# Kernel optimization log

Hardware: AMD Instinct MI355X
Metric: run time of the kernel (lower is better)

Reference implementation:

```python
import jax, jax.numpy as jnp
from jax import lax
import numpy as np

B, C, H, W = 1, 128, 32, 32
OC, K = 128, 3
STRIDE, PAD, DIL = 1, 1, 1
ARRAY_SIZE = 32
QUANT = 8


def setup_inputs() -> dict:
    key = jax.random.key(0)
    k1, k2, k3 = jax.random.split(key, 3)
    x = jax.random.normal(k1, (B, C, H, W), dtype=jnp.float32)
    weight = jax.random.normal(k2, (OC, C, K, K), dtype=jnp.float32) * 0.05
    bias = jax.random.normal(k3, (OC,), dtype=jnp.float32) * 0.05
    return {"x": x, "weight": weight, "bias": bias}


def _conv(x, w, b):
    out = lax.conv_general_dilated(
        x, w, window_strides=(STRIDE, STRIDE),
        padding=((PAD, PAD), (PAD, PAD)),
        rhs_dilation=(DIL, DIL),
        dimension_numbers=("NCHW", "OIHW", "NCHW"))
    return out + b[None, :, None, None]


def _unfold(x, oh, ow):
    # torch F.unfold: (B, C*K*K, L) with channel-major ordering (c, kh, kw)
    xp = jnp.pad(x, ((0, 0), (0, 0), (PAD, PAD), (PAD, PAD)))
    cols = jnp.stack(
        [xp[:, :, i:i + oh, j:j + ow] for i in range(K) for j in range(K)],
        axis=2)  # (B, C, K*K, OH, OW)
    return cols.reshape(B, C * K * K, oh * ow)


def reference(x, weight, bias):
    oh = (H + 2 * PAD - DIL * (K - 1) - 1) // STRIDE + 1
    ow = (W + 2 * PAD - DIL * (K - 1) - 1) // STRIDE + 1
    L = oh * ow
    qmax = float(2 ** QUANT - 1)

    # --- set_quant_params: per-spatial-location scale/zero_point from full conv out ---
    out_full = _conv(x, weight, bias).reshape(1, OC, -1)  # (1, OC, L)
    mx = jnp.max(out_full, axis=1)  # (1, L)
    mn = jnp.min(out_full, axis=1)
    scale = (mx - mn) / qmax
    zp = jnp.clip(-mn / scale, 0.0, qmax)
    zp = jnp.where(jnp.isnan(zp), 0.0, zp)
    zp = jnp.trunc(zp)  # .int() truncation
    scale = lax.stop_gradient(scale)[:, None, None, :]  # (1,1,1,L)
    zp = lax.stop_gradient(zp)[:, None, None, :]

    # --- unfold + explicit elementwise multiply (crossbar expansion) ---
    cols = _unfold(x, oh, ow)                       # (B, C*K*K, L)
    pre = cols[:, None, :, :] * weight.reshape(1, OC, C * K * K, 1)  # (B,OC,CKK,L)

    # pad front of dim 2 to a multiple of array_size (pads a full chunk if divisible)
    ckk = C * K * K
    pad_d3 = ARRAY_SIZE - ckk % ARRAY_SIZE
    pre = jnp.pad(pre, ((0, 0), (0, 0), (pad_d3, 0), (0, 0)))

    # block-sum over array_size chunks (crossbar partial sums)
    n_chunks = (ckk + pad_d3) // ARRAY_SIZE
    accu = pre.reshape(B, OC, n_chunks, ARRAY_SIZE, L).sum(axis=3)  # (B,OC,n_chunks,L)

    # per-chunk fake-quant (Quant8F) with straight-through estimator
    q = jnp.clip(jnp.round(accu / scale) + zp, 0.0, qmax)
    deq = (q - zp) * scale
    quant_accu = accu + lax.stop_gradient(deq - accu)

    # reduce over chunks -> conv output (note: bias is NOT added in original forward)
    return quant_accu.sum(axis=2).reshape(B, OC, oh, ow)
```

## Files before the change

### kernel.cpp

```cpp
#include <hip/hip_runtime.h>

#define L_     1024
#define CKK_   1152
#define QMAX_  255.0f
#define NCH    36
#define PLANE_ 131072

__global__ __launch_bounds__(256) void gemm_chunks(
    const float* __restrict__ x,
    const float* __restrict__ w,
    float* __restrict__ planes)
{
    __shared__ __align__(16) float Ws[8][32];
    const int t      = threadIdx.x;
    const int ocBase = blockIdx.x * 8;
    const int l      = blockIdx.y * 256 + t;
    const int j      = blockIdx.z;
    const int oh     = l >> 5, ow = l & 31;
    const int d0     = j * 32;

    const int  s_oc = t >> 5, s_k = t & 31;
    const float wval = w[(ocBase + s_oc) * CKK_ + d0 + s_k];

    float xv[32];
#pragma unroll
    for (int dd = 0; dd < 32; dd++) {
        const int d  = d0 + dd;
        const int c  = d / 9;
        const int r  = d - 9 * c;
        const int kh = r / 3;
        const int kw = r - 3 * kh;
        const int off = c * 1024 + (kh - 1) * 32 + (kw - 1);
        const bool ok = ((unsigned)(oh + kh - 1) < 32u) &
                        ((unsigned)(ow + kw - 1) < 32u);
        const int idx = ok ? (off + l) : 0;
        const float vv = x[idx];
        xv[dd] = ok ? vv : 0.f;
    }

    Ws[s_oc][s_k] = wval;
    __syncthreads();

    float acc[8];
#pragma unroll
    for (int oc = 0; oc < 8; oc++) {
        const float4* wp = (const float4*)&Ws[oc][0];
        float pa = 0.f, pb = 0.f;
#pragma unroll
        for (int k4 = 0; k4 < 4; k4++) {
            const float4 wv = wp[k4];
            pa = fmaf(wv.x, xv[4 * k4 + 0], pa);
            pa = fmaf(wv.y, xv[4 * k4 + 1], pa);
            pa = fmaf(wv.z, xv[4 * k4 + 2], pa);
            pa = fmaf(wv.w, xv[4 * k4 + 3], pa);
        }
#pragma unroll
        for (int k4 = 4; k4 < 8; k4++) {
            const float4 wv = wp[k4];
            pb = fmaf(wv.x, xv[4 * k4 + 0], pb);
            pb = fmaf(wv.y, xv[4 * k4 + 1], pb);
            pb = fmaf(wv.z, xv[4 * k4 + 2], pb);
            pb = fmaf(wv.w, xv[4 * k4 + 3], pb);
        }
        acc[oc] = pa + pb;
    }

    float* dst = planes + (size_t)j * PLANE_ + (size_t)l * 128 + ocBase;
    *(float4*)(dst + 0) = make_float4(acc[0], acc[1], acc[2], acc[3]);
    *(float4*)(dst + 4) = make_float4(acc[4], acc[5], acc[6], acc[7]);
}

__global__ __launch_bounds__(256) void fused_mq(
    const float* __restrict__ planes,
    const float* __restrict__ bias,
    float* __restrict__ out)
{
    __shared__ float part[256];
    __shared__ float mnb[128], mxb[128];
    __shared__ float s_sc, s_zp, s_iv;
    const int t  = threadIdx.x;
    const int oc = t & 127, jh = t >> 7;
    const int l  = blockIdx.x;

    const float* p = planes + (size_t)(jh * 18) * PLANE_ + (size_t)l * 128 + oc;
    float v[18];
#pragma unroll
    for (int j = 0; j < 18; j++) v[j] = p[(size_t)j * PLANE_];

    float s = 0.f;
#pragma unroll
    for (int j = 0; j < 18; j++) s += v[j];
    part[t] = s;
    __syncthreads();

    if (t < 128) {
        const float tot = part[t] + part[t + 128] + bias[t];
        mnb[t] = tot;
        mxb[t] = tot;
    }
    __syncthreads();
#pragma unroll
    for (int st = 64; st > 0; st >>= 1) {
        if (t < st) {
            mnb[t] = fminf(mnb[t], mnb[t + st]);
            mxb[t] = fmaxf(mxb[t], mxb[t + st]);
        }
        __syncthreads();
    }
    if (t == 0) {
        const float amn = mnb[0], amx = mxb[0];
        const float sv  = (amx - amn) / QMAX_;
        float z = -amn / sv;
        z = fmaxf(z, 0.f);
        z = fminf(z, QMAX_);
        z = truncf(z);
        s_sc = sv;
        s_zp = z;
        s_iv = 1.0f / sv;
    }
    __syncthreads();

    const float sc = s_sc, zv = s_zp, iv = s_iv;
    float q = 0.f;
#pragma unroll
    for (int j = 0; j < 18; j++) {
        float qn = rintf(v[j] * iv) + zv;
        qn = fminf(fmaxf(qn, 0.f), QMAX_);
        q += (qn - zv) * sc;
    }
    part[t] = q;
    __syncthreads();

    if (t < 128)
        out[oc * L_ + l] = part[t] + part[t + 128];
}

template <bool QUANT>
__global__ __launch_bounds__(256) void cas_direct(
    const float* __restrict__ x, const float* __restrict__ w,
    float* __restrict__ out, const float* __restrict__ scale,
    const float* __restrict__ zp, const float* __restrict__ inv)
{
    const int t = threadIdx.x;
    const int ocBase = blockIdx.x * 16;
    const int l = blockIdx.y * 256 + t;
    const int oh = l >> 5, ow = l & 31;

    float sc = 0.f, zv = 0.f, iv = 0.f;
    if (QUANT) { sc = scale[l]; zv = zp[l]; iv = inv[l]; }

    float acc[16];
#pragma unroll
    for (int oc = 0; oc < 16; oc++) acc[oc] = 0.f;

    for (int j = 0; j < NCH; j++) {
        const int d0 = j * 32;
        float xv[32];
#pragma unroll
        for (int dd = 0; dd < 32; dd++) {
            const int d = d0 + dd, c = d / 9, r = d - 9 * c;
            const int kh = r / 3, kw = r - 3 * kh;
            const int off = c * 1024 + (kh - 1) * 32 + (kw - 1);
            const bool ok = ((unsigned)(oh + kh - 1) < 32u) &
                            ((unsigned)(ow + kw - 1) < 32u);
            const int idx = ok ? (off + l) : 0;
            const float vv = x[idx];
            xv[dd] = ok ? vv : 0.f;
        }
#pragma unroll
        for (int oc = 0; oc < 16; oc++) {
            const float4* wp = (const float4*)(w + (ocBase + oc) * CKK_ + d0);
            float pa = 0.f, pb = 0.f;
#pragma unroll
            for (int k4 = 0; k4 < 8; k4++) {
                const float4 wv = wp[k4];
                float& pr = (k4 < 4) ? pa : pb;
                pr = fmaf(wv.x, xv[4 * k4 + 0], pr);
                pr = fmaf(wv.y, xv[4 * k4 + 1], pr);
                pr = fmaf(wv.z, xv[4 * k4 + 2], pr);
                pr = fmaf(wv.w, xv[4 * k4 + 3], pr);
            }
            const float s2 = pa + pb;
            if (QUANT) {
                float qn = rintf(s2 * iv) + zv;
                qn = fminf(fmaxf(qn, 0.f), QMAX_);
                acc[oc] += (qn - zv) * sc;
            } else {
                acc[oc] += s2;
            }
        }
    }
#pragma unroll
    for (int oc = 0; oc < 16; oc++)
        out[(ocBase + oc) * L_ + l] = acc[oc];
}

__global__ __launch_bounds__(256) void minmax_conv(
    const float* __restrict__ conv, const float* __restrict__ bias,
    float* __restrict__ scale, float* __restrict__ zp, float* __restrict__ inv)
{
    __shared__ float smn[16][17], smx[16][17];
    const int t = threadIdx.x, li = t & 15, g = t >> 4;
    const int l = blockIdx.x * 16 + li;
    float mn = INFINITY, mx = -INFINITY;
#pragma unroll
    for (int i = 0; i < 8; i++) {
        const int oc = g * 8 + i;
        const float v = conv[oc * L_ + l] + bias[oc];
        mn = fminf(mn, v); mx = fmaxf(mx, v);
    }
    smn[g][li] = mn; smx[g][li] = mx;
    __syncthreads();
    if (t < 16) {
        const int l2 = blockIdx.x * 16 + t;
        float amn = smn[0][t], amx = smx[0][t];
#pragma unroll
        for (int g2 = 1; g2 < 16; g2++) {
            amn = fminf(amn, smn[g2][t]); amx = fmaxf(amx, smx[g2][t]);
        }
        const float s = (amx - amn) / QMAX_;
        float z = -amn / s;
        z = fminf(fmaxf(z, 0.f), QMAX_);
        z = truncf(z);
        scale[l2] = s; zp[l2] = z; inv[l2] = 1.0f / s;
    }
}

extern "C" void kernel_launch(void* const* d_in, const int* in_sizes, int n_in,
                              void* d_out, int out_size, void* d_ws, size_t ws_size,
                              hipStream_t stream) {
    const float* x    = (const float*)d_in[0];
    const float* w    = (const float*)d_in[1];
    const float* bias = (const float*)d_in[2];
    float* out = (float*)d_out;
    float* ws  = (float*)d_ws;

    const size_t main_need = (size_t)NCH * PLANE_ * 4;
    if (ws_size >= main_need) {
        float* planes = ws;
        gemm_chunks<<<dim3(16, 4, NCH), 256, 0, stream>>>(x, w, planes);
        fused_mq<<<1024, 256, 0, stream>>>(planes, bias, out);
    } else {
        float* conv  = ws;
        float* scale = conv + PLANE_;
        float* zpv   = scale + 1024;
        float* inv   = zpv + 1024;
        cas_direct<false><<<dim3(8, 4), 256, 0, stream>>>(x, w, conv, nullptr, nullptr, nullptr);
        minmax_conv<<<64, 256, 0, stream>>>(conv, bias, scale, zpv, inv);
        cas_direct<true><<<dim3(8, 4), 256, 0, stream>>>(x, w, out, scale, zpv, inv);
    }
}
```

Baseline: 82.38 us.

## Retile chunk GEMM with shared-memory x and weight tiles and register blocking

The per-chunk GEMM kernel now stages a 32x128 weight slice (transposed) and a 32x64 im2col tile of x in shared memory. Each thread computes a 4x8 register tile of output channels by spatial positions. Previously every block re-gathered 32 x values per thread for only 8 output channels, so x reads and address math were repeated across 16 oc-blocks. The new layout cuts redundant global gathers and raises FMA-to-load ratio. The cost is fewer, larger blocks (576 vs 2304) and more shared memory per block.

New measurement: 75.92 us. 7.8% less time.

```diff
diff --git a/kernel.cpp b/kernel.cpp
--- a/kernel.cpp
+++ b/kernel.cpp
@@ -11,63 +11,107 @@
     const float* __restrict__ w,
     float* __restrict__ planes)
 {
-    __shared__ __align__(16) float Ws[8][32];
-    const int t      = threadIdx.x;
-    const int ocBase = blockIdx.x * 8;
-    const int l      = blockIdx.y * 256 + t;
-    const int j      = blockIdx.z;
-    const int oh     = l >> 5, ow = l & 31;
-    const int d0     = j * 32;
-
-    const int  s_oc = t >> 5, s_k = t & 31;
-    const float wval = w[(ocBase + s_oc) * CKK_ + d0 + s_k];
-
-    float xv[32];
-#pragma unroll
-    for (int dd = 0; dd < 32; dd++) {
-        const int d  = d0 + dd;
-        const int c  = d / 9;
-        const int r  = d - 9 * c;
-        const int kh = r / 3;
-        const int kw = r - 3 * kh;
-        const int off = c * 1024 + (kh - 1) * 32 + (kw - 1);
-        const bool ok = ((unsigned)(oh + kh - 1) < 32u) &
-                        ((unsigned)(ow + kw - 1) < 32u);
-        const int idx = ok ? (off + l) : 0;
-        const float vv = x[idx];
-        xv[dd] = ok ? vv : 0.f;
-    }
-
-    Ws[s_oc][s_k] = wval;
-    __syncthreads();
-
-    float acc[8];
-#pragma unroll
-    for (int oc = 0; oc < 8; oc++) {
-        const float4* wp = (const float4*)&Ws[oc][0];
-        float pa = 0.f, pb = 0.f;
-#pragma unroll
-        for (int k4 = 0; k4 < 4; k4++) {
-            const float4 wv = wp[k4];
-            pa = fmaf(wv.x, xv[4 * k4 + 0], pa);
-            pa = fmaf(wv.y, xv[4 * k4 + 1], pa);
-            pa = fmaf(wv.z, xv[4 * k4 + 2], pa);
-            pa = fmaf(wv.w, xv[4 * k4 + 3], pa);
-        }
-#pragma unroll
-        for (int k4 = 4; k4 < 8; k4++) {
-            const float4 wv = wp[k4];
-            pb = fmaf(wv.x, xv[4 * k4 + 0], pb);
-            pb = fmaf(wv.y, xv[4 * k4 + 1], pb);
-            pb = fmaf(wv.z, xv[4 * k4 + 2], pb);
-            pb = fmaf(wv.w, xv[4 * k4 + 3], pb);
-        }
-        acc[oc] = pa + pb;
-    }
-
-    float* dst = planes + (size_t)j * PLANE_ + (size_t)l * 128 + ocBase;
-    *(float4*)(dst + 0) = make_float4(acc[0], acc[1], acc[2], acc[3]);
-    *(float4*)(dst + 4) = make_float4(acc[4], acc[5], acc[6], acc[7]);
+    __shared__ __align__(16) float Wb[32][132];
+    __shared__ __align__(16) float xs[32][64];
+
+    const int t   = threadIdx.x;
+    const int l0  = blockIdx.x * 64;
+    const int j   = blockIdx.y;
+    const int d0  = j * 32;
+    const int oh0 = l0 >> 5;
+
+    float4 wld[4];
+    int    wo[4], wk[4];
+#pragma unroll
+    for (int it = 0; it < 4; it++) {
+        const int f4 = it * 256 + t;
+        wo[it]  = f4 >> 3;
+        wk[it]  = (f4 & 7) * 4;
+        wld[it] = *(const float4*)(w + wo[it] * CKK_ + d0 + wk[it]);
+    }
+
+    float xl[8];
+    int   xk[8], xll[8];
+#pragma unroll
+    for (int it = 0; it < 8; it++) {
+        const int e  = it * 256 + t;
+        const int k  = e >> 6, ll = e & 63;
+        const int d  = d0 + k;
+        const int c  = d / 9, r = d - 9 * c;
+        const int kh = r / 3, kw = r - 3 * kh;
+        const int iy = oh0 + (ll >> 5) + kh - 1;
+        const int ix = (ll & 31) + kw - 1;
+        const bool ok = ((unsigned)iy < 32u) & ((unsigned)ix < 32u);
+        const int idx = ok ? (c * 1024 + iy * 32 + ix) : 0;
+        const float v = x[idx];
+        xl[it] = ok ? v : 0.f;
+        xk[it] = k; xll[it] = ll;
+    }
+
+#pragma unroll
+    for (int it = 0; it < 4; it++) {
+        Wb[wk[it] + 0][wo[it]] = wld[it].x;
+        Wb[wk[it] + 1][wo[it]] = wld[it].y;
+        Wb[wk[it] + 2][wo[it]] = wld[it].z;
+        Wb[wk[it] + 3][wo[it]] = wld[it].w;
+    }
+#pragma unroll
+    for (int it = 0; it < 8; it++)
+        xs[xk[it]][xll[it]] = xl[it];
+    __syncthreads();
+
+    const int oc0 = (t & 31) * 4;
+    const int ll0 = (t >> 5) * 8;
+    float acc[4][8];
+#pragma unroll
+    for (int r = 0; r < 4; r++)
+#pragma unroll
+        for (int i = 0; i < 8; i++) acc[r][i] = 0.f;
+
+#pragma unroll
+    for (int k = 0; k < 32; k++) {
+        const float4 wv = *(const float4*)&Wb[k][oc0];
+        const float4 xa = *(const float4*)&xs[k][ll0];
+        const float4 xb = *(const float4*)&xs[k][ll0 + 4];
+        acc[0][0] = fmaf(wv.x, xa.x, acc[0][0]);
+        acc[0][1] = fmaf(wv.x, xa.y, acc[0][1]);
+        acc[0][2] = fmaf(wv.x, xa.z, acc[0][2]);
+        acc[0][3] = fmaf(wv.x, xa.w, acc[0][3]);
+        acc[0][4] = fmaf(wv.x, xb.x, acc[0][4]);
+        acc[0][5] = fmaf(wv.x, xb.y, acc[0][5]);
+        acc[0][6] = fmaf(wv.x, xb.z, acc[0][6]);
+        acc[0][7] = fmaf(wv.x, xb.w, acc[0][7]);
+        acc[1][0] = fmaf(wv.y, xa.x, acc[1][0]);
+        acc[1][1] = fmaf(wv.y, xa.y, acc[1][1]);
+        acc[1][2] = fmaf(wv.y, xa.z, acc[1][2]);
+        acc[1][3] = fmaf(wv.y, xa.w, acc[1][3]);
+        acc[1][4] = fmaf(wv.y, xb.x, acc[1][4]);
+        acc[1][5] = fmaf(wv.y, xb.y, acc[1][5]);
+        acc[1][6] = fmaf(wv.y, xb.z, acc[1][6]);
+        acc[1][7] = fmaf(wv.y, xb.w, acc[1][7]);
+        acc[2][0] = fmaf(wv.z, xa.x, acc[2][0]);
+        acc[2][1] = fmaf(wv.z, xa.y, acc[2][1]);
+        acc[2][2] = fmaf(wv.z, xa.z, acc[2][2]);
+        acc[2][3] = fmaf(wv.z, xa.w, acc[2][3]);
+        acc[2][4] = fmaf(wv.z, xb.x, acc[2][4]);
+        acc[2][5] = fmaf(wv.z, xb.y, acc[2][5]);
+        acc[2][6] = fmaf(wv.z, xb.z, acc[2][6]);
+        acc[2][7] = fmaf(wv.z, xb.w, acc[2][7]);
+        acc[3][0] = fmaf(wv.w, xa.x, acc[3][0]);
+        acc[3][1] = fmaf(wv.w, xa.y, acc[3][1]);
+        acc[3][2] = fmaf(wv.w, xa.z, acc[3][2]);
+        acc[3][3] = fmaf(wv.w, xa.w, acc[3][3]);
+        acc[3][4] = fmaf(wv.w, xb.x, acc[3][4]);
+        acc[3][5] = fmaf(wv.w, xb.y, acc[3][5]);
+        acc[3][6] = fmaf(wv.w, xb.z, acc[3][6]);
+        acc[3][7] = fmaf(wv.w, xb.w, acc[3][7]);
+    }
+
+    float* dst = planes + (size_t)j * PLANE_ + (size_t)l0 * 128;
+#pragma unroll
+    for (int i = 0; i < 8; i++)
+        *(float4*)(dst + (ll0 + i) * 128 + oc0) =
+            make_float4(acc[0][i], acc[1][i], acc[2][i], acc[3][i]);
 }
 
 __global__ __launch_bounds__(256) void fused_mq(
@@ -238,7 +282,7 @@
     const size_t main_need = (size_t)NCH * PLANE_ * 4;
     if (ws_size >= main_need) {
         float* planes = ws;
-        gemm_chunks<<<dim3(16, 4, NCH), 256, 0, stream>>>(x, w, planes);
+        gemm_chunks<<<dim3(16, NCH), 256, 0, stream>>>(x, w, planes);
         fused_mq<<<1024, 256, 0, stream>>>(planes, bias, out);
     } else {
         float* conv  = ws;
```
